# Kernel optimization log

Measured on AMD Instinct MI355X. Metric: run time of the kernel, lower is better.

The kernel has to match this reference:

```python
import jax, jax.numpy as jnp
import numpy as np
from jax import lax
import math

B = 4
T = 8000          # audio samples
T_MEL = 32        # mel frames
N_IN = 256        # mu-law classes
L = 16            # n_layers
MAX_DIL = 128
R = 64            # n_residual_channels
S = 256           # n_skip_channels
O = 256           # n_out_channels
CC = 80           # n_cond_channels
UP_W = 1024
UP_S = 256
LOOP = int(math.floor(math.log2(MAX_DIL))) + 1  # 8


def setup_inputs() -> dict:
    key = jax.random.key(0)
    ks = jax.random.split(key, 16)
    s = 0.05
    return {
        "features": jax.random.normal(ks[0], (B, CC, T_MEL), jnp.float32),
        "forward_input": jax.random.randint(ks[1], (B, T), 0, N_IN),
        "embed": jax.random.normal(ks[2], (N_IN, R), jnp.float32) * s,
        # torch ConvTranspose1d weight layout: (in, out, k)
        "up_w": jax.random.normal(ks[3], (CC, CC, UP_W), jnp.float32) * s,
        "up_b": jax.random.normal(ks[4], (CC,), jnp.float32) * s,
        "cond_w": jax.random.normal(ks[5], (2 * R * L, CC), jnp.float32) * s,
        "cond_b": jax.random.normal(ks[6], (2 * R * L,), jnp.float32) * s,
        "dil_w": jax.random.normal(ks[7], (L, 2 * R, R, 2), jnp.float32) * s,
        "dil_b": jax.random.normal(ks[8], (L, 2 * R), jnp.float32) * s,
        "res_w": jax.random.normal(ks[9], (L - 1, R, R), jnp.float32) * s,
        "res_b": jax.random.normal(ks[10], (L - 1, R), jnp.float32) * s,
        "skip_w": jax.random.normal(ks[11], (L, S, R), jnp.float32) * s,
        "skip_b": jax.random.normal(ks[12], (L, S), jnp.float32) * s,
        "conv_out_w": jax.random.normal(ks[13], (O, S), jnp.float32) * s,
        "conv_end_w": jax.random.normal(ks[14], (O, O), jnp.float32) * s,
    }


def _wavenet(features, forward_input, embed, up_w, up_b, cond_w, cond_b,
             dil_w, dil_b, res_w, res_b, skip_w, skip_b, conv_out_w, conv_end_w):
    # conditioning upsample: ConvTranspose1d, out len = (T_mel-1)*stride + window
    cond = lax.conv_transpose(
        features, up_w, strides=(UP_S,), padding='VALID',
        dimension_numbers=('NCH', 'IOH', 'NCH'), transpose_kernel=True)
    cond = cond + up_b[None, :, None]
    cond = cond[:, :, :T]  # truncate to audio length

    x = embed[forward_input].transpose(0, 2, 1)  # [B, R, T]
    cond_acts = jnp.einsum('oi,bit->bot', cond_w, cond) + cond_b[None, :, None]

    output = None
    for i in range(L):
        d = 2 ** (i % LOOP)
        # causal dilated conv, kernel=2: left-pad by dilation
        xp = jnp.pad(x, ((0, 0), (0, 0), (d, 0)))
        in_act = lax.conv_general_dilated(
            xp, dil_w[i], window_strides=(1,), padding='VALID',
            rhs_dilation=(d,), dimension_numbers=('NCH', 'OIH', 'NCH'))
        in_act = in_act + dil_b[i][None, :, None]
        in_act = in_act + cond_acts[:, i * 2 * R:(i + 1) * 2 * R, :]
        acts = jnp.tanh(in_act[:, :R, :]) * jax.nn.sigmoid(in_act[:, R:, :])
        if i < L - 1:
            x = jnp.einsum('oi,bit->bot', res_w[i], acts) + res_b[i][None, :, None] + x
        skip = jnp.einsum('oi,bit->bot', skip_w[i], acts) + skip_b[i][None, :, None]
        output = skip if output is None else output + skip

    output = jax.nn.relu(output)
    output = jnp.einsum('oi,bit->bot', conv_out_w, output)
    output = jax.nn.relu(output)
    output = jnp.einsum('oi,bit->bot', conv_end_w, output)
    # shift right by one, first frame zeroed
    output = jnp.concatenate(
        [jnp.zeros_like(output[:, :, :1]), output[:, :, :-1]], axis=2)
    return output


def reference(features, forward_input, embed, up_w, up_b, cond_w, cond_b,
              dil_w, dil_b, res_w, res_b, skip_w, skip_b, conv_out_w, conv_end_w):
    return _wavenet(features, forward_input, embed, up_w, up_b, cond_w, cond_b,
                    dil_w, dil_b, res_w, res_b, skip_w, skip_b,
                    conv_out_w, conv_end_w)
```

## Files before the change

kernel.cpp:

```cpp
#include <hip/hip_runtime.h>
#include <cstdint>

#define TT 8000
#define NB 4

typedef _Float16 half8 __attribute__((ext_vector_type(8)));
typedef float f32x4 __attribute__((ext_vector_type(4)));

static __device__ __forceinline__ f32x4 MFMA16(half8 a, half8 b, f32x4 c){
  return __builtin_amdgcn_mfma_f32_16x16x32_f16(a, b, c, 0, 0, 0);
}

static __device__ __forceinline__ float gatef(float a, float b){
  a = fminf(fmaxf(a, -20.f), 20.f);
  float e2a = __expf(2.f*a);
  float th = __fdividef(e2a - 1.f, e2a + 1.f);
  float sg = __fdividef(1.f, 1.f + __expf(-b));
  return th * sg;
}

union PK4 { uint64_t u; _Float16 h[4]; };

__global__ void prep_kernel(const float* __restrict__ dil_w, const float* __restrict__ cond_w,
                            const float* __restrict__ res_w, const float* __restrict__ skip_w,
                            const float* __restrict__ cow, const float* __restrict__ cew,
                            const float* __restrict__ skip_b,
                            _Float16* __restrict__ WdT, _Float16* __restrict__ Wc,
                            _Float16* __restrict__ Wr, _Float16* __restrict__ Wsa,
                            _Float16* __restrict__ Wco, _Float16* __restrict__ Wce,
                            float* __restrict__ bsum)
{
  int g = blockIdx.x*256 + threadIdx.x;
  if (g < 262144){
    int r = g & 63, m = (g>>6) & 127, tap = (g>>13) & 1, l = g>>14;
    WdT[g] = (_Float16)dil_w[(((l*128+m)*64 + r)*2) + tap];
  } else if ((g -= 262144) < 196608){
    int o = g % 96; int rest = g / 96; int m = rest & 127; int l = rest >> 7;
    Wc[g] = (_Float16)((o < 80) ? cond_w[(l*128+m)*80 + o] : 0.f);
  } else if ((g -= 196608) < 61440){
    Wr[g] = (_Float16)res_w[g];
  } else if ((g -= 61440) < 262144){
    int kk = g & 1023, m = g >> 10; int l = kk >> 6, j = kk & 63;
    Wsa[g] = (_Float16)skip_w[(l*256+m)*64 + j];
  } else if ((g -= 262144) < 65536){
    Wco[g] = (_Float16)cow[g];
  } else if ((g -= 65536) < 65536){
    Wce[g] = (_Float16)cew[g];
  } else if ((g -= 65536) < 256){
    float s = 0.f;
    for (int l = 0; l < 16; l++) s += skip_b[l*256 + g];
    bsum[g] = s;
  }
}

__global__ __launch_bounds__(256) void upsample_kernel(
    const float* __restrict__ feat, const float* __restrict__ up_w,
    const float* __restrict__ up_b, float* __restrict__ condf)
{
  int tc = blockIdx.x, o = blockIdx.y, tid = threadIdx.x;
  int t = tc*256 + tid;
  float ub = up_b[o];
  float a0 = ub, a1 = ub, a2 = ub, a3 = ub;
  #pragma unroll
  for (int ds = 0; ds < 4; ds++){
    int s = tc - ds;
    if (s >= 0){
      const float* wb = up_w + (size_t)o*81920 + 256*ds + tid;
      const float* fb = feat + s;
      for (int i = 0; i < 80; i++){
        float wv = wb[(size_t)i*1024];
        a0 = __fmaf_rn(wv, fb[(size_t)(0*80+i)*32], a0);
        a1 = __fmaf_rn(wv, fb[(size_t)(1*80+i)*32], a1);
        a2 = __fmaf_rn(wv, fb[(size_t)(2*80+i)*32], a2);
        a3 = __fmaf_rn(wv, fb[(size_t)(3*80+i)*32], a3);
      }
    }
  }
  if (t < TT){
    condf[((size_t)(0*80+o))*TT + t] = a0;
    condf[((size_t)(1*80+o))*TT + t] = a1;
    condf[((size_t)(2*80+o))*TT + t] = a2;
    condf[((size_t)(3*80+o))*TT + t] = a3;
  }
}

__global__ __launch_bounds__(256) void condpack_kernel(
    const float* __restrict__ condf, _Float16* __restrict__ condh)
{
  __shared__ float ls[64*101];
  int t0 = blockIdx.x*64, n = blockIdx.y, tid = threadIdx.x;
  for (int e = tid; e < 5120; e += 256){
    int ch = e >> 6, tl = e & 63;
    ls[tl*101 + ch] = condf[((size_t)(n*80+ch))*TT + t0 + tl];
  }
  __syncthreads();
  uint32_t* dst = (uint32_t*)condh;
  for (int e = tid; e < 3072; e += 256){
    int tl = e / 48, cp = e % 48; int c0 = cp*2;
    float f0 = (c0   < 80) ? ls[tl*101 + c0]   : 0.f;
    float f1 = (c0+1 < 80) ? ls[tl*101 + c0+1] : 0.f;
    _Float16 h0 = (_Float16)f0, h1 = (_Float16)f1;
    uint16_t u0 = *(uint16_t*)&h0, u1 = *(uint16_t*)&h1;
    dst[((size_t)n*TT + t0 + tl)*48 + cp] = ((uint32_t)u1 << 16) | u0;
  }
}

__global__ __launch_bounds__(256) void embed_kernel(
    const int* __restrict__ fi, const float* __restrict__ embed, float* __restrict__ x)
{
  int tile = blockIdx.x; int n = blockIdx.y;
  int lane = threadIdx.x & 63, grp = threadIdx.x >> 6;
  int t = tile*64 + lane;
  int idx = fi[(size_t)n*TT + t];
  const float* er = embed + (size_t)idx*64 + grp*16;
  float* xp = x + ((size_t)n*64 + grp*16)*TT + t;
  #pragma unroll
  for (int r = 0; r < 16; r++) xp[(size_t)r*TT] = er[r];
}

template<bool LAST>
__global__ __launch_bounds__(256) void layer_mfma(
    const float* __restrict__ xin, float* __restrict__ xout,
    const _Float16* __restrict__ condh,
    _Float16* __restrict__ actsL,
    const _Float16* __restrict__ WdT,
    const _Float16* __restrict__ Wc,
    const _Float16* __restrict__ Wr,
    const float* __restrict__ dil_b_l,
    const float* __restrict__ cond_b_l,
    const float* __restrict__ res_b_l,
    int d)
{
  __shared__ __attribute__((aligned(16))) char als[8192];
  int bx = blockIdx.x;
  int tile = bx % 125, n = bx / 125;
  int tid = threadIdx.x;
  int lane = tid & 63;
  int w = tid >> 6;
  int t0 = tile*64;
  int l16 = lane & 15;
  int lg  = lane >> 4;
  const float* xn = xin + (size_t)n*64*TT;

  half8 aD[2][2][2];
  half8 aC[2][3];
  #pragma unroll
  for (int mi = 0; mi < 2; mi++){
    int m = (w + 4*mi)*16 + l16;
    #pragma unroll
    for (int tap = 0; tap < 2; tap++)
      #pragma unroll
      for (int ks = 0; ks < 2; ks++)
        aD[tap][mi][ks] = *(const half8*)(WdT + ((size_t)(tap*128 + m)*64 + ks*32 + lg*8));
    #pragma unroll
    for (int kc = 0; kc < 3; kc++)
      aC[mi][kc] = *(const half8*)(Wc + ((size_t)m*96 + kc*32 + lg*8));
  }
  float bias[2][4];
  #pragma unroll
  for (int mi = 0; mi < 2; mi++)
    #pragma unroll
    for (int r = 0; r < 4; r++){
      int mm = (w + 4*mi)*16 + lg*4 + r;
      bias[mi][r] = dil_b_l[mm] + cond_b_l[mm];
    }

  f32x4 acc[2][4];
  #pragma unroll
  for (int nt = 0; nt < 4; nt++){
    int t = t0 + nt*16 + l16;
    int td = t - d;
    half8 bcur[2], bdel[2], bcnd[3];
    #pragma unroll
    for (int ks = 0; ks < 2; ks++){
      const float* xc = xn + (size_t)(ks*32 + lg*8)*TT + t;
      #pragma unroll
      for (int j = 0; j < 8; j++) bcur[ks][j] = (_Float16)xc[(size_t)j*TT];
      const float* xd = xn + (size_t)(ks*32 + lg*8)*TT + td;
      #pragma unroll
      for (int j = 0; j < 8; j++) bdel[ks][j] = (_Float16)((td >= 0) ? xd[(size_t)j*TT] : 0.f);
    }
    #pragma unroll
    for (int kc = 0; kc < 3; kc++)
      bcnd[kc] = *(const half8*)(condh + ((size_t)n*TT + t)*96 + kc*32 + lg*8);

    #pragma unroll
    for (int mi = 0; mi < 2; mi++){
      f32x4 a; a[0]=bias[mi][0]; a[1]=bias[mi][1]; a[2]=bias[mi][2]; a[3]=bias[mi][3];
      a = MFMA16(aD[0][mi][0], bdel[0], a);
      a = MFMA16(aD[0][mi][1], bdel[1], a);
      a = MFMA16(aD[1][mi][0], bcur[0], a);
      a = MFMA16(aD[1][mi][1], bcur[1], a);
      a = MFMA16(aC[mi][0], bcnd[0], a);
      a = MFMA16(aC[mi][1], bcnd[1], a);
      a = MFMA16(aC[mi][2], bcnd[2], a);
      acc[mi][nt] = a;
    }
  }

  int ch0 = w*16 + lg*4;
  #pragma unroll
  for (int nt = 0; nt < 4; nt++){
    int tl = nt*16 + l16;
    PK4 pk;
    #pragma unroll
    for (int r = 0; r < 4; r++)
      pk.h[r] = (_Float16)gatef(acc[0][nt][r], acc[1][nt][r]);
    if (!LAST)
      *(uint64_t*)(als + tl*128 + ((ch0*2) ^ ((tl & 7) << 4))) = pk.u;
    *(uint64_t*)(actsL + ((size_t)n*TT + t0 + tl)*1024 + ch0) = pk.u;
  }

  if (!LAST){
    __syncthreads();
    half8 aR[2];
    int mr = w*16 + l16;
    #pragma unroll
    for (int ks = 0; ks < 2; ks++)
      aR[ks] = *(const half8*)(Wr + (size_t)mr*64 + ks*32 + lg*8);
    float rb[4];
    #pragma unroll
    for (int r = 0; r < 4; r++) rb[r] = res_b_l[w*16 + lg*4 + r];
    float* xo = xout + (size_t)n*64*TT;
    #pragma unroll
    for (int nt = 0; nt < 4; nt++){
      int tl = nt*16 + l16; int t = t0 + tl;
      half8 bA[2];
      #pragma unroll
      for (int ks = 0; ks < 2; ks++)
        bA[ks] = *(const half8*)(als + tl*128 + (((ks*32 + lg*8)*2) ^ ((tl & 7) << 4)));
      f32x4 rc; rc[0]=rb[0]; rc[1]=rb[1]; rc[2]=rb[2]; rc[3]=rb[3];
      rc = MFMA16(aR[0], bA[0], rc);
      rc = MFMA16(aR[1], bA[1], rc);
      #pragma unroll
      for (int r = 0; r < 4; r++){
        int m = w*16 + lg*4 + r;
        xo[(size_t)m*TT + t] = rc[r] + xn[(size_t)m*TT + t];
      }
    }
  }
}

__global__ __launch_bounds__(256) void final_fused(
    const _Float16* __restrict__ actsG,
    const _Float16* __restrict__ Wsa,
    const _Float16* __restrict__ Wco,
    const _Float16* __restrict__ Wce,
    const float* __restrict__ bsum,
    float* __restrict__ out)
{
  __shared__ __attribute__((aligned(16))) char ls[32768];
  int bx = blockIdx.x;
  int tile = bx % 125, n = bx / 125;
  int tid = threadIdx.x;
  int lane = tid & 63;
  int w = tid >> 6;
  int t0 = tile*64;
  int l16 = lane & 15;
  int lg  = lane >> 4;

  f32x4 acc[4][4];
  #pragma unroll
  for (int mi = 0; mi < 4; mi++)
    #pragma unroll
    for (int nt = 0; nt < 4; nt++){
      f32x4 a;
      #pragma unroll
      for (int r = 0; r < 4; r++) a[r] = bsum[(4*w+mi)*16 + lg*4 + r];
      acc[mi][nt] = a;
    }
  for (int ks = 0; ks < 32; ks++){
    half8 bf[4];
    #pragma unroll
    for (int nt = 0; nt < 4; nt++){
      int t = t0 + nt*16 + l16;
      bf[nt] = *(const half8*)(actsG + ((size_t)n*TT + t)*1024 + ks*32 + lg*8);
    }
    #pragma unroll
    for (int mi = 0; mi < 4; mi++){
      int m = (4*w+mi)*16 + l16;
      half8 af = *(const half8*)(Wsa + (size_t)m*1024 + ks*32 + lg*8);
      #pragma unroll
      for (int nt = 0; nt < 4; nt++) acc[mi][nt] = MFMA16(af, bf[nt], acc[mi][nt]);
    }
  }
  #pragma unroll
  for (int mi = 0; mi < 4; mi++){
    int c0 = (4*w+mi)*16 + lg*4;
    #pragma unroll
    for (int nt = 0; nt < 4; nt++){
      int tl = nt*16 + l16;
      PK4 pk;
      #pragma unroll
      for (int r = 0; r < 4; r++) pk.h[r] = (_Float16)fmaxf(acc[mi][nt][r], 0.f);
      *(uint64_t*)(ls + tl*512 + ((c0*2) ^ ((tl & 7) << 4))) = pk.u;
    }
  }
  __syncthreads();

  #pragma unroll
  for (int mi = 0; mi < 4; mi++)
    #pragma unroll
    for (int nt = 0; nt < 4; nt++){ f32x4 a; a[0]=0;a[1]=0;a[2]=0;a[3]=0; acc[mi][nt]=a; }
  #pragma unroll
  for (int ks = 0; ks < 8; ks++){
    half8 bf[4];
    #pragma unroll
    for (int nt = 0; nt < 4; nt++){
      int tl = nt*16 + l16;
      bf[nt] = *(const half8*)(ls + tl*512 + (((ks*32 + lg*8)*2) ^ ((tl & 7) << 4)));
    }
    #pragma unroll
    for (int mi = 0; mi < 4; mi++){
      int m = (4*w+mi)*16 + l16;
      half8 af = *(const half8*)(Wco + (size_t)m*256 + ks*32 + lg*8);
      #pragma unroll
      for (int nt = 0; nt < 4; nt++) acc[mi][nt] = MFMA16(af, bf[nt], acc[mi][nt]);
    }
  }
  __syncthreads();
  #pragma unroll
  for (int mi = 0; mi < 4; mi++){
    int c0 = (4*w+mi)*16 + lg*4;
    #pragma unroll
    for (int nt = 0; nt < 4; nt++){
      int tl = nt*16 + l16;
      PK4 pk;
      #pragma unroll
      for (int r = 0; r < 4; r++) pk.h[r] = (_Float16)fmaxf(acc[mi][nt][r], 0.f);
      *(uint64_t*)(ls + tl*512 + ((c0*2) ^ ((tl & 7) << 4))) = pk.u;
    }
  }
  __syncthreads();

  #pragma unroll
  for (int mi = 0; mi < 4; mi++)
    #pragma unroll
    for (int nt = 0; nt < 4; nt++){ f32x4 a; a[0]=0;a[1]=0;a[2]=0;a[3]=0; acc[mi][nt]=a; }
  #pragma unroll
  for (int ks = 0; ks < 8; ks++){
    half8 bf[4];
    #pragma unroll
    for (int nt = 0; nt < 4; nt++){
      int tl = nt*16 + l16;
      bf[nt] = *(const half8*)(ls + tl*512 + (((ks*32 + lg*8)*2) ^ ((tl & 7) << 4)));
    }
    #pragma unroll
    for (int mi = 0; mi < 4; mi++){
      int m = (4*w+mi)*16 + l16;
      half8 af = *(const half8*)(Wce + (size_t)m*256 + ks*32 + lg*8);
      #pragma unroll
      for (int nt = 0; nt < 4; nt++) acc[mi][nt] = MFMA16(af, bf[nt], acc[mi][nt]);
    }
  }
  #pragma unroll
  for (int mi = 0; mi < 4; mi++)
    #pragma unroll
    for (int nt = 0; nt < 4; nt++)
      #pragma unroll
      for (int r = 0; r < 4; r++){
        int m = (4*w+mi)*16 + lg*4 + r;
        int t = t0 + nt*16 + l16;
        size_t ob = ((size_t)n*256 + m)*TT;
        if (t + 1 < TT) out[ob + t + 1] = acc[mi][nt][r];
        if (t == 0)     out[ob] = 0.f;
      }
}

extern "C" void kernel_launch(void* const* d_in, const int* in_sizes, int n_in,
                              void* d_out, int out_size, void* d_ws, size_t ws_size,
                              hipStream_t stream)
{
  const float* feat   = (const float*)d_in[0];
  const int*   fi     = (const int*)  d_in[1];
  const float* embed  = (const float*)d_in[2];
  const float* up_w   = (const float*)d_in[3];
  const float* up_b   = (const float*)d_in[4];
  const float* cond_w = (const float*)d_in[5];
  const float* cond_b = (const float*)d_in[6];
  const float* dil_w  = (const float*)d_in[7];
  const float* dil_b  = (const float*)d_in[8];
  const float* res_w  = (const float*)d_in[9];
  const float* res_b  = (const float*)d_in[10];
  const float* skip_w = (const float*)d_in[11];
  const float* skip_b = (const float*)d_in[12];
  const float* cow    = (const float*)d_in[13];
  const float* cew    = (const float*)d_in[14];
  float* out = (float*)d_out;
  float* cur = (float*)d_ws;

  float*     xA    = cur;               cur += 2048000;
  float*     xB    = cur;               cur += 2048000;
  _Float16*  condh = (_Float16*)cur;    cur += 1536000;
  _Float16*  WdT   = (_Float16*)cur;    cur += 131072;
  _Float16*  Wc    = (_Float16*)cur;    cur += 98304;
  _Float16*  Wr    = (_Float16*)cur;    cur += 30720;
  _Float16*  Wsa   = (_Float16*)cur;    cur += 131072;
  _Float16*  Wco   = (_Float16*)cur;    cur += 32768;
  _Float16*  Wce   = (_Float16*)cur;    cur += 32768;
  float*     bsum  = cur;               cur += 256;
  _Float16*  actsG = (_Float16*)cur;
  float*     condf = cur;

  prep_kernel<<<3569, 256, 0, stream>>>(dil_w, cond_w, res_w, skip_w, cow, cew, skip_b,
                                        WdT, Wc, Wr, Wsa, Wco, Wce, bsum);
  upsample_kernel<<<dim3(32,80), 256, 0, stream>>>(feat, up_w, up_b, condf);
  condpack_kernel<<<dim3(125,4), 256, 0, stream>>>(condf, condh);
  embed_kernel<<<dim3(125,4), 256, 0, stream>>>(fi, embed, xA);

  const float* xin = xA; float* xout = xB;
  for (int l = 0; l < 16; l++){
    int dd = 1 << (l & 7);
    const _Float16* WdTl = WdT + (size_t)l*16384;
    const _Float16* Wcl  = Wc  + (size_t)l*12288;
    const _Float16* Wrl  = Wr  + (size_t)(l < 15 ? l : 0)*4096;
    const float*    rbl  = res_b + (size_t)(l < 15 ? l : 0)*64;
    _Float16* actsL = actsG + (size_t)l*64;
    if (l == 15)
      layer_mfma<true><<<500, 256, 0, stream>>>((const float*)xin, xout, condh, actsL,
          WdTl, Wcl, Wrl, dil_b + l*128, cond_b + l*128, rbl, dd);
    else
      layer_mfma<false><<<500, 256, 0, stream>>>((const float*)xin, xout, condh, actsL,
          WdTl, Wcl, Wrl, dil_b + l*128, cond_b + l*128, rbl, dd);
    const float* nin = xout; xout = (float*)xin; xin = nin;
  }

  final_fused<<<500, 256, 0, stream>>>(actsG, Wsa, Wco, Wce, bsum, out);
}
```

Before: 600.3 us.

## Store residual state time-major with an fp16 shadow copy; retile upsample and final kernel

The residual stream moves from channel-major fp32 to time-major layout. A separate fp16 copy is kept so each layer reads the current and delayed inputs as contiguous half8 vectors instead of strided scalar fp32 loads. The fp32 residual is updated in place with a 4-wide vector read-modify-write, and the fp16 copy is double-buffered. Separately, the upsample kernel now computes four time chunks per thread to reuse each weight load, and final_fused uses 512 threads with two M-tiles per wave and a wider LDS swizzle. The cost is extra writes for the fp16 copy, plus fewer upsample blocks and higher register pressure in the reworked kernels.

```diff
diff --git a/kernel.cpp b/kernel.cpp
--- a/kernel.cpp
+++ b/kernel.cpp
@@ -58,29 +58,38 @@
     const float* __restrict__ up_b, float* __restrict__ condf)
 {
   int tc = blockIdx.x, o = blockIdx.y, tid = threadIdx.x;
-  int t = tc*256 + tid;
   float ub = up_b[o];
-  float a0 = ub, a1 = ub, a2 = ub, a3 = ub;
+  float acc[4][4];
+  #pragma unroll
+  for (int q = 0; q < 4; q++)
+    #pragma unroll
+    for (int n = 0; n < 4; n++) acc[q][n] = ub;
+
   #pragma unroll
   for (int ds = 0; ds < 4; ds++){
-    int s = tc - ds;
-    if (s >= 0){
-      const float* wb = up_w + (size_t)o*81920 + 256*ds + tid;
-      const float* fb = feat + s;
-      for (int i = 0; i < 80; i++){
-        float wv = wb[(size_t)i*1024];
-        a0 = __fmaf_rn(wv, fb[(size_t)(0*80+i)*32], a0);
-        a1 = __fmaf_rn(wv, fb[(size_t)(1*80+i)*32], a1);
-        a2 = __fmaf_rn(wv, fb[(size_t)(2*80+i)*32], a2);
-        a3 = __fmaf_rn(wv, fb[(size_t)(3*80+i)*32], a3);
+    const float* wb = up_w + (size_t)o*81920 + 256*ds + tid;
+    for (int i = 0; i < 80; i++){
+      float wv = wb[(size_t)i*1024];
+      #pragma unroll
+      for (int q = 0; q < 4; q++){
+        int s = 4*tc + q - ds;
+        if (s >= 0){
+          const float* fb = feat + (size_t)i*32 + s;
+          #pragma unroll
+          for (int n = 0; n < 4; n++)
+            acc[q][n] = __fmaf_rn(wv, fb[(size_t)n*2560], acc[q][n]);
+        }
       }
     }
   }
-  if (t < TT){
-    condf[((size_t)(0*80+o))*TT + t] = a0;
-    condf[((size_t)(1*80+o))*TT + t] = a1;
-    condf[((size_t)(2*80+o))*TT + t] = a2;
-    condf[((size_t)(3*80+o))*TT + t] = a3;
+  #pragma unroll
+  for (int q = 0; q < 4; q++){
+    int t = tc*1024 + q*256 + tid;
+    if (t < TT){
+      #pragma unroll
+      for (int n = 0; n < 4; n++)
+        condf[((size_t)(n*80+o))*TT + t] = acc[q][n];
+    }
   }
 }
 
@@ -106,21 +115,29 @@
 }
 
 __global__ __launch_bounds__(256) void embed_kernel(
-    const int* __restrict__ fi, const float* __restrict__ embed, float* __restrict__ x)
-{
-  int tile = blockIdx.x; int n = blockIdx.y;
-  int lane = threadIdx.x & 63, grp = threadIdx.x >> 6;
-  int t = tile*64 + lane;
+    const int* __restrict__ fi, const float* __restrict__ embed,
+    float* __restrict__ xf, _Float16* __restrict__ xh)
+{
+  int tile = blockIdx.x, n = blockIdx.y;
+  int tl = threadIdx.x >> 2, g = threadIdx.x & 3;
+  int t = tile*64 + tl;
   int idx = fi[(size_t)n*TT + t];
-  const float* er = embed + (size_t)idx*64 + grp*16;
-  float* xp = x + ((size_t)n*64 + grp*16)*TT + t;
-  #pragma unroll
-  for (int r = 0; r < 16; r++) xp[(size_t)r*TT] = er[r];
+  const float* er = embed + (size_t)idx*64 + g*16;
+  float* xo = xf + ((size_t)n*TT + t)*64 + g*16;
+  _Float16* ho = xh + ((size_t)n*TT + t)*64 + g*16;
+  #pragma unroll
+  for (int r = 0; r < 16; r++){
+    float v = er[r];
+    xo[r] = v;
+    ho[r] = (_Float16)v;
+  }
 }
 
 template<bool LAST>
 __global__ __launch_bounds__(256) void layer_mfma(
-    const float* __restrict__ xin, float* __restrict__ xout,
+    float* __restrict__ xf,
+    const _Float16* __restrict__ xh_in,
+    _Float16* __restrict__ xh_out,
     const _Float16* __restrict__ condh,
     _Float16* __restrict__ actsL,
     const _Float16* __restrict__ WdT,
@@ -140,7 +157,7 @@
   int t0 = tile*64;
   int l16 = lane & 15;
   int lg  = lane >> 4;
-  const float* xn = xin + (size_t)n*64*TT;
+  const _Float16* xhn = xh_in + (size_t)n*TT*64;
 
   half8 aD[2][2][2];
   half8 aC[2][3];
@@ -172,13 +189,17 @@
     int td = t - d;
     half8 bcur[2], bdel[2], bcnd[3];
     #pragma unroll
-    for (int ks = 0; ks < 2; ks++){
-      const float* xc = xn + (size_t)(ks*32 + lg*8)*TT + t;
-      #pragma unroll
-      for (int j = 0; j < 8; j++) bcur[ks][j] = (_Float16)xc[(size_t)j*TT];
-      const float* xd = xn + (size_t)(ks*32 + lg*8)*TT + td;
-      #pragma unroll
-      for (int j = 0; j < 8; j++) bdel[ks][j] = (_Float16)((td >= 0) ? xd[(size_t)j*TT] : 0.f);
+    for (int ks = 0; ks < 2; ks++)
+      bcur[ks] = *(const half8*)(xhn + (size_t)t*64 + ks*32 + lg*8);
+    if (td >= 0){
+      #pragma unroll
+      for (int ks = 0; ks < 2; ks++)
+        bdel[ks] = *(const half8*)(xhn + (size_t)td*64 + ks*32 + lg*8);
+    } else {
+      #pragma unroll
+      for (int ks = 0; ks < 2; ks++)
+        #pragma unroll
+        for (int j = 0; j < 8; j++) bdel[ks][j] = (_Float16)0.f;
     }
     #pragma unroll
     for (int kc = 0; kc < 3; kc++)
@@ -221,7 +242,6 @@
     float rb[4];
     #pragma unroll
     for (int r = 0; r < 4; r++) rb[r] = res_b_l[w*16 + lg*4 + r];
-    float* xo = xout + (size_t)n*64*TT;
     #pragma unroll
     for (int nt = 0; nt < 4; nt++){
       int tl = nt*16 + l16; int t = t0 + tl;
@@ -232,16 +252,19 @@
       f32x4 rc; rc[0]=rb[0]; rc[1]=rb[1]; rc[2]=rb[2]; rc[3]=rb[3];
       rc = MFMA16(aR[0], bA[0], rc);
       rc = MFMA16(aR[1], bA[1], rc);
-      #pragma unroll
-      for (int r = 0; r < 4; r++){
-        int m = w*16 + lg*4 + r;
-        xo[(size_t)m*TT + t] = rc[r] + xn[(size_t)m*TT + t];
-      }
-    }
-  }
-}
-
-__global__ __launch_bounds__(256) void final_fused(
+      float* xp = xf + ((size_t)n*TT + t)*64 + w*16 + lg*4;
+      f32x4 xv = *(const f32x4*)xp;
+      xv += rc;
+      *(f32x4*)xp = xv;
+      PK4 pk;
+      #pragma unroll
+      for (int r = 0; r < 4; r++) pk.h[r] = (_Float16)xv[r];
+      *(uint64_t*)(xh_out + ((size_t)n*TT + t)*64 + w*16 + lg*4) = pk.u;
+    }
+  }
+}
+
+__global__ __launch_bounds__(512) void final_fused(
     const _Float16* __restrict__ actsG,
     const _Float16* __restrict__ Wsa,
     const _Float16* __restrict__ Wco,
@@ -259,14 +282,14 @@
   int l16 = lane & 15;
   int lg  = lane >> 4;
 
-  f32x4 acc[4][4];
-  #pragma unroll
-  for (int mi = 0; mi < 4; mi++)
+  f32x4 acc[2][4];
+  #pragma unroll
+  for (int mi = 0; mi < 2; mi++)
     #pragma unroll
     for (int nt = 0; nt < 4; nt++){
       f32x4 a;
       #pragma unroll
-      for (int r = 0; r < 4; r++) a[r] = bsum[(4*w+mi)*16 + lg*4 + r];
+      for (int r = 0; r < 4; r++) a[r] = bsum[(2*w+mi)*16 + lg*4 + r];
       acc[mi][nt] = a;
     }
   for (int ks = 0; ks < 32; ks++){
@@ -277,29 +300,29 @@
       bf[nt] = *(const half8*)(actsG + ((size_t)n*TT + t)*1024 + ks*32 + lg*8);
     }
     #pragma unroll
-    for (int mi = 0; mi < 4; mi++){
-      int m = (4*w+mi)*16 + l16;
+    for (int mi = 0; mi < 2; mi++){
+      int m = (2*w+mi)*16 + l16;
       half8 af = *(const half8*)(Wsa + (size_t)m*1024 + ks*32 + lg*8);
       #pragma unroll
       for (int nt = 0; nt < 4; nt++) acc[mi][nt] = MFMA16(af, bf[nt], acc[mi][nt]);
     }
   }
   #pragma unroll
-  for (int mi = 0; mi < 4; mi++){
-    int c0 = (4*w+mi)*16 + lg*4;
+  for (int mi = 0; mi < 2; mi++){
+    int c0 = (2*w+mi)*16 + lg*4;
     #pragma unroll
     for (int nt = 0; nt < 4; nt++){
       int tl = nt*16 + l16;
       PK4 pk;
       #pragma unroll
       for (int r = 0; r < 4; r++) pk.h[r] = (_Float16)fmaxf(acc[mi][nt][r], 0.f);
-      *(uint64_t*)(ls + tl*512 + ((c0*2) ^ ((tl & 7) << 4))) = pk.u;
+      *(uint64_t*)(ls + tl*512 + ((c0*2) ^ ((tl & 15) << 4))) = pk.u;
     }
   }
   __syncthreads();
 
   #pragma unroll
-  for (int mi = 0; mi < 4; mi++)
+  for (int mi = 0; mi < 2; mi++)
     #pragma unroll
     for (int nt = 0; nt < 4; nt++){ f32x4 a; a[0]=0;a[1]=0;a[2]=0;a[3]=0; acc[mi][nt]=a; }
   #pragma unroll
@@ -308,11 +331,11 @@
     #pragma unroll
     for (int nt = 0; nt < 4; nt++){
       int tl = nt*16 + l16;
-      bf[nt] = *(const half8*)(ls + tl*512 + (((ks*32 + lg*8)*2) ^ ((tl & 7) << 4)));
-    }
-    #pragma unroll
-    for (int mi = 0; mi < 4; mi++){
-      int m = (4*w+mi)*16 + l16;
+      bf[nt] = *(const half8*)(ls + tl*512 + (((ks*32 + lg*8)*2) ^ ((tl & 15) << 4)));
+    }
+    #pragma unroll
+    for (int mi = 0; mi < 2; mi++){
+      int m = (2*w+mi)*16 + l16;
       half8 af = *(const half8*)(Wco + (size_t)m*256 + ks*32 + lg*8);
       #pragma unroll
       for (int nt = 0; nt < 4; nt++) acc[mi][nt] = MFMA16(af, bf[nt], acc[mi][nt]);
@@ -320,21 +343,21 @@
   }
   __syncthreads();
   #pragma unroll
-  for (int mi = 0; mi < 4; mi++){
-    int c0 = (4*w+mi)*16 + lg*4;
+  for (int mi = 0; mi < 2; mi++){
+    int c0 = (2*w+mi)*16 + lg*4;
     #pragma unroll
     for (int nt = 0; nt < 4; nt++){
       int tl = nt*16 + l16;
       PK4 pk;
       #pragma unroll
       for (int r = 0; r < 4; r++) pk.h[r] = (_Float16)fmaxf(acc[mi][nt][r], 0.f);
-      *(uint64_t*)(ls + tl*512 + ((c0*2) ^ ((tl & 7) << 4))) = pk.u;
+      *(uint64_t*)(ls + tl*512 + ((c0*2) ^ ((tl & 15) << 4))) = pk.u;
     }
   }
   __syncthreads();
 
   #pragma unroll
-  for (int mi = 0; mi < 4; mi++)
+  for (int mi = 0; mi < 2; mi++)
     #pragma unroll
     for (int nt = 0; nt < 4; nt++){ f32x4 a; a[0]=0;a[1]=0;a[2]=0;a[3]=0; acc[mi][nt]=a; }
   #pragma unroll
@@ -343,23 +366,23 @@
     #pragma unroll
     for (int nt = 0; nt < 4; nt++){
       int tl = nt*16 + l16;
-      bf[nt] = *(const half8*)(ls + tl*512 + (((ks*32 + lg*8)*2) ^ ((tl & 7) << 4)));
-    }
-    #pragma unroll
-    for (int mi = 0; mi < 4; mi++){
-      int m = (4*w+mi)*16 + l16;
+      bf[nt] = *(const half8*)(ls + tl*512 + (((ks*32 + lg*8)*2) ^ ((tl & 15) << 4)));
+    }
+    #pragma unroll
+    for (int mi = 0; mi < 2; mi++){
+      int m = (2*w+mi)*16 + l16;
       half8 af = *(const half8*)(Wce + (size_t)m*256 + ks*32 + lg*8);
       #pragma unroll
       for (int nt = 0; nt < 4; nt++) acc[mi][nt] = MFMA16(af, bf[nt], acc[mi][nt]);
     }
   }
   #pragma unroll
-  for (int mi = 0; mi < 4; mi++)
+  for (int mi = 0; mi < 2; mi++)
     #pragma unroll
     for (int nt = 0; nt < 4; nt++)
       #pragma unroll
       for (int r = 0; r < 4; r++){
-        int m = (4*w+mi)*16 + lg*4 + r;
+        int m = (2*w+mi)*16 + lg*4 + r;
         int t = t0 + nt*16 + l16;
         size_t ob = ((size_t)n*256 + m)*TT;
         if (t + 1 < TT) out[ob + t + 1] = acc[mi][nt][r];
@@ -389,8 +412,9 @@
   float* out = (float*)d_out;
   float* cur = (float*)d_ws;
 
-  float*     xA    = cur;               cur += 2048000;
-  float*     xB    = cur;               cur += 2048000;
+  float*     xf    = cur;               cur += 2048000;
+  _Float16*  xhA   = (_Float16*)cur;    cur += 1024000;
+  _Float16*  xhB   = (_Float16*)cur;    cur += 1024000;
   _Float16*  condh = (_Float16*)cur;    cur += 1536000;
   _Float16*  WdT   = (_Float16*)cur;    cur += 131072;
   _Float16*  Wc    = (_Float16*)cur;    cur += 98304;
@@ -404,11 +428,11 @@
 
   prep_kernel<<<3569, 256, 0, stream>>>(dil_w, cond_w, res_w, skip_w, cow, cew, skip_b,
                                         WdT, Wc, Wr, Wsa, Wco, Wce, bsum);
-  upsample_kernel<<<dim3(32,80), 256, 0, stream>>>(feat, up_w, up_b, condf);
+  upsample_kernel<<<dim3(8,80), 256, 0, stream>>>(feat, up_w, up_b, condf);
   condpack_kernel<<<dim3(125,4), 256, 0, stream>>>(condf, condh);
-  embed_kernel<<<dim3(125,4), 256, 0, stream>>>(fi, embed, xA);
-
-  const float* xin = xA; float* xout = xB;
+  embed_kernel<<<dim3(125,4), 256, 0, stream>>>(fi, embed, xf, xhA);
+
+  const _Float16* xhin = xhA; _Float16* xhout = xhB;
   for (int l = 0; l < 16; l++){
     int dd = 1 << (l & 7);
     const _Float16* WdTl = WdT + (size_t)l*16384;
@@ -417,13 +441,13 @@
     const float*    rbl  = res_b + (size_t)(l < 15 ? l : 0)*64;
     _Float16* actsL = actsG + (size_t)l*64;
     if (l == 15)
-      layer_mfma<true><<<500, 256, 0, stream>>>((const float*)xin, xout, condh, actsL,
+      layer_mfma<true><<<500, 256, 0, stream>>>(xf, xhin, xhout, condh, actsL,
           WdTl, Wcl, Wrl, dil_b + l*128, cond_b + l*128, rbl, dd);
     else
-      layer_mfma<false><<<500, 256, 0, stream>>>((const float*)xin, xout, condh, actsL,
+      layer_mfma<false><<<500, 256, 0, stream>>>(xf, xhin, xhout, condh, actsL,
           WdTl, Wcl, Wrl, dil_b + l*128, cond_b + l*128, rbl, dd);
-    const float* nin = xout; xout = (float*)xin; xin = nin;
-  }
-
-  final_fused<<<500, 256, 0, stream>>>(actsG, Wsa, Wco, Wce, bsum, out);
-}
+    const _Float16* nin = xhout; xhout = (_Float16*)xhin; xhin = nin;
+  }
+
+  final_fused<<<500, 512, 0, stream>>>(actsG, Wsa, Wco, Wce, bsum, out);
+}
```

After: 659.2 us. 9.8% more time.
